# Optimization experiments

Measured on AMD Instinct MI355X. Metric: run time of the kernel, lower is better.

## Reference

```python
import jax, jax.numpy as jnp
import numpy as np

B, N, E, D, AD = 8, 1000, 4, 64, 32  # batch, n_node, n_edge_types, state_dim, annotation_dim
W_SCALE = 0.02  # matches normal_(0.0, 0.02) init


def setup_inputs() -> dict:
    key = jax.random.key(0)
    ks = jax.random.split(key, 10)
    return {
        "prop_state": jax.random.normal(ks[0], (B, N, D), jnp.float32),
        "annotation": jax.random.normal(ks[1], (B, N, AD), jnp.float32),
        "A": jax.random.uniform(ks[2], (B, N, 2 * N * E), jnp.float32),
        "W_in": W_SCALE * jax.random.normal(ks[3], (E, D, D), jnp.float32),
        "W_out": W_SCALE * jax.random.normal(ks[4], (E, D, D), jnp.float32),
        "W_r": W_SCALE * jax.random.normal(ks[5], (D, 3 * D), jnp.float32),
        "W_z": W_SCALE * jax.random.normal(ks[6], (D, 3 * D), jnp.float32),
        "W_h": W_SCALE * jax.random.normal(ks[7], (D, 3 * D), jnp.float32),
        "Wo1": W_SCALE * jax.random.normal(ks[8], (D, D + AD), jnp.float32),
        "Wo2": W_SCALE * jax.random.normal(ks[9], (1, D), jnp.float32),
    }


def _propagate(state, A_in, A_out, W_in, W_out, W_r, W_z, W_h):
    b, n, d = state.shape
    e = W_in.shape[0]
    # per-edge-type linear transforms (torch Linear: y = x @ W.T), batched over edge types
    # layout matches torch: stack over e then transpose(0,1) -> [b, e, n, d] -> [b, e*n, d]
    s_in = jnp.einsum('bnd,efd->benf', state, W_in).reshape(b, e * n, d)
    s_out = jnp.einsum('bnd,efd->benf', state, W_out).reshape(b, e * n, d)
    a_in = jnp.matmul(A_in, s_in)    # [b, n, d]
    a_out = jnp.matmul(A_out, s_out)  # [b, n, d]
    a = jnp.concatenate([a_in, a_out, state], axis=2)  # [b, n, 3d]
    r = jax.nn.sigmoid(a @ W_r.T)
    z = jax.nn.sigmoid(a @ W_z.T)
    joined = jnp.concatenate([a_in, a_out, r * state], axis=2)
    h_hat = jnp.tanh(joined @ W_h.T)
    return (1.0 - z) * state + z * h_hat


def reference(prop_state, annotation, A, W_in, W_out, W_r, W_z, W_h, Wo1, Wo2):
    n = prop_state.shape[1]
    e = W_in.shape[0]
    ne = n * e
    A_in, A_out = A[:, :, :ne], A[:, :, ne:]
    # exactly two propagation steps (n_steps_flag path in the original)
    s1 = _propagate(prop_state, A_in, A_out, W_in, W_out, W_r, W_z, W_h)
    s2 = _propagate(s1, A_in, A_out, W_in, W_out, W_r, W_z, W_h)
    join_state = jnp.concatenate([s2, annotation], axis=2)  # [b, n, d+ad]
    out = jnp.tanh(join_state @ Wo1.T) @ Wo2.T  # [b, n, 1]
    return out.sum(axis=2)  # [b, n]
```

## Files before the change

### kernel.cpp

```cpp
#include <hip/hip_runtime.h>


typedef float  f32x4_t  __attribute__((ext_vector_type(4)));
typedef __bf16 bf16x8_t __attribute__((ext_vector_type(8)));
typedef __bf16 bf16x4_t __attribute__((ext_vector_type(4)));

#define MFMA16(a, b, c) __builtin_amdgcn_mfma_f32_16x16x32_bf16((a), (b), (c), 0, 0, 0)

static constexpr int kN   = 1000;
static constexpr int kD   = 64;
static constexpr int kAD  = 32;
static constexpr int kPb  = 8000 * 64;
static constexpr int kPl  = 5;

__device__ __forceinline__ float4 ld4(const float* p) {
    return *reinterpret_cast<const float4*>(p);
}

__device__ __forceinline__ bf16x8_t cvt8(float4 a, float4 b) {
    bf16x8_t r;
    r[0] = (__bf16)a.x; r[1] = (__bf16)a.y; r[2] = (__bf16)a.z; r[3] = (__bf16)a.w;
    r[4] = (__bf16)b.x; r[5] = (__bf16)b.y; r[6] = (__bf16)b.z; r[7] = (__bf16)b.w;
    return r;
}

__device__ __forceinline__ bf16x8_t sum5pb(const __bf16* p) {
    float s0 = 0.f, s1 = 0.f, s2 = 0.f, s3 = 0.f;
    float s4 = 0.f, s5 = 0.f, s6 = 0.f, s7 = 0.f;
    #pragma unroll
    for (int pl = 0; pl < kPl; ++pl) {
        const bf16x8_t v = *reinterpret_cast<const bf16x8_t*>(p + (size_t)pl * kPb);
        s0 += (float)v[0]; s1 += (float)v[1]; s2 += (float)v[2]; s3 += (float)v[3];
        s4 += (float)v[4]; s5 += (float)v[5]; s6 += (float)v[6]; s7 += (float)v[7];
    }
    bf16x8_t r;
    r[0] = (__bf16)s0; r[1] = (__bf16)s1; r[2] = (__bf16)s2; r[3] = (__bf16)s3;
    r[4] = (__bf16)s4; r[5] = (__bf16)s5; r[6] = (__bf16)s6; r[7] = (__bf16)s7;
    return r;
}

__device__ __forceinline__ float sigm(float x) {
    x = fminf(fmaxf(x, -30.f), 30.f);
    return 1.0f / (1.0f + __expf(-x));
}

__device__ __forceinline__ float fast_tanh(float x) {
    x = fminf(fmaxf(x, -15.f), 15.f);
    const float e = __expf(-2.0f * x);
    return (1.0f - e) / (1.0f + e);
}

__global__ __launch_bounds__(256) void precompute_swt(
    const float* __restrict__ state,
    const float* __restrict__ W_in,
    const float* __restrict__ W_out,
    __bf16* __restrict__ SWTfrag)
{
    const int bx = blockIdx.x;
    const int jt = bx & 15;
    const int e  = (bx >> 4) & 3;
    const int h  = (bx >> 6) & 1;
    const int b  = bx >> 7;
    const float* W = (h ? W_out : W_in) + e * kD * kD;

    const int tid  = threadIdx.x;
    const int w    = tid >> 6;
    const int lane = tid & 63;
    const int m    = lane & 15;
    const int q    = lane >> 4;

    __shared__ __bf16 T[64][72];

    const int  jj    = jt * 64 + w * 16 + m;
    const bool valid = (jj < kN);
    const float* srow = state + ((size_t)b * kN + (valid ? jj : kN - 1)) * kD + q * 8;
    float4 a0 = ld4(srow),      a1 = ld4(srow + 4);
    float4 a2 = ld4(srow + 32), a3 = ld4(srow + 36);
    if (!valid) {
        a0 = make_float4(0.f, 0.f, 0.f, 0.f); a1 = a0; a2 = a0; a3 = a0;
    }
    const bf16x8_t af0 = cvt8(a0, a1);
    const bf16x8_t af1 = cvt8(a2, a3);

    #pragma unroll
    for (int c = 0; c < 4; ++c) {
        const int f = c * 16 + m;
        const float* wrow = W + f * kD + q * 8;
        const bf16x8_t bf0 = cvt8(ld4(wrow),      ld4(wrow + 4));
        const bf16x8_t bf1 = cvt8(ld4(wrow + 32), ld4(wrow + 36));
        f32x4_t acc = {0.f, 0.f, 0.f, 0.f};
        acc = MFMA16(af0, bf0, acc);
        acc = MFMA16(af1, bf1, acc);
        const int j0 = w * 16 + q * 4;
        bf16x4_t v;
        v[0] = (__bf16)acc[0]; v[1] = (__bf16)acc[1];
        v[2] = (__bf16)acc[2]; v[3] = (__bf16)acc[3];
        *reinterpret_cast<bf16x4_t*>(&T[f][j0]) = v;
    }
    __syncthreads();

    const int bh = b * 2 + h;
    #pragma unroll
    for (int rep = 0; rep < 2; ++rep) {
        const int m2 = tid & 15;
        const int cc = (tid >> 4) & 3;
        const int ol = (tid >> 6) + rep * 4;
        const int j0 = jt * 64 + ol * 8;
        if (j0 < kN) {
            const int jg = e * kN + j0;
            const int s  = jg >> 5;
            const int qq = (jg >> 3) & 3;
            const uint4 v = *reinterpret_cast<uint4*>(&T[cc * 16 + m2][ol * 8]);
            const size_t el = ((((size_t)bh * 125 + s) * 4 + cc) * 64 + qq * 16 + m2) * 8;
            *reinterpret_cast<uint4*>((__bf16*)SWTfrag + el) = v;
        }
    }
}

__global__ __launch_bounds__(256, 4) void fused_mm1(
    const float* __restrict__ A,
    const __bf16* __restrict__ SWTfrag,
    __bf16* __restrict__ Afrag,
    __bf16* __restrict__ a_in_p,
    __bf16* __restrict__ a_out_p)
{
    const int bx   = blockIdx.x;
    const int tile = bx & 15;
    const int rest = bx >> 4;
    const int kseg = rest % 5;
    const int rhb  = rest / 5;
    const int h    = rhb & 1;
    const int b    = rhb >> 1;

    const int t    = threadIdx.x;
    const int wv   = t >> 6;
    const int lane = t & 63;
    const int m    = lane & 15;
    const int q    = lane >> 4;

    __shared__ __bf16 L[2][64][136];

    const float* Abase = A + (size_t)b * kN * 8000 + h * 4000;
    const int bh = b * 2 + h;

    f32x4_t acc0 = {0.f, 0.f, 0.f, 0.f};
    f32x4_t acc1 = {0.f, 0.f, 0.f, 0.f};
    f32x4_t acc2 = {0.f, 0.f, 0.f, 0.f};
    f32x4_t acc3 = {0.f, 0.f, 0.f, 0.f};

    const __bf16* pBbase = SWTfrag + (size_t)bh * 125 * 2048 + (size_t)lane * 8;
    __bf16* pAout = Afrag +
        ((((size_t)(bh * 64 + tile * 4 + wv)) * 125) * 64 + lane) * 8;

    float4 ra[4][2];

    auto load_chunk = [&](int c, bool tail) {
        const int kabs = kseg * 800 + c * 128;
        #pragma unroll
        for (int p = 0; p < 4; ++p) {
            if (p == 0 || !tail) {
                const int idx = p * 256 + t;
                const int r   = tail ? (t >> 2) : (idx >> 4);
                const int c8  = tail ? (t & 3)  : (idx & 15);
                int i = tile * 64 + r;
                if (i >= kN) i = kN - 1;
                const float* src = Abase + (size_t)i * 8000 + kabs + c8 * 8;
                ra[p][0] = ld4(src);
                ra[p][1] = ld4(src + 4);
            }
        }
    };
    auto write_chunk = [&](int buf, bool tail) {
        #pragma unroll
        for (int p = 0; p < 4; ++p) {
            if (p == 0 || !tail) {
                const int idx = p * 256 + t;
                const int r   = tail ? (t >> 2) : (idx >> 4);
                const int c8  = tail ? (t & 3)  : (idx & 15);
                *reinterpret_cast<bf16x8_t*>(&L[buf][r][c8 * 8]) =
                    cvt8(ra[p][0], ra[p][1]);
            }
        }
    };
    auto compute_chunk = [&](int c, int nst, int buf) {
        #pragma unroll
        for (int sp = 0; sp < 4; ++sp) {
            if (sp < nst) {
                const int s = kseg * 25 + c * 4 + sp;
                const bf16x8_t af =
                    *reinterpret_cast<const bf16x8_t*>(&L[buf][wv * 16 + m][sp * 32 + q * 8]);
                *reinterpret_cast<bf16x8_t*>(pAout + (size_t)s * 512) = af;

                const __bf16* pB = pBbase + (size_t)s * 2048;
                const bf16x8_t b0 = *(const bf16x8_t*)(pB);
                const bf16x8_t b1 = *(const bf16x8_t*)(pB + 512);
                const bf16x8_t b2 = *(const bf16x8_t*)(pB + 1024);
                const bf16x8_t b3 = *(const bf16x8_t*)(pB + 1536);
                acc0 = MFMA16(af, b0, acc0);
                acc1 = MFMA16(af, b1, acc1);
                acc2 = MFMA16(af, b2, acc2);
                acc3 = MFMA16(af, b3, acc3);
            }
        }
    };

    load_chunk(0, false);
    write_chunk(0, false);
    __syncthreads();
    load_chunk(1, false);

    #pragma unroll 1
    for (int c = 0; c < 6; ++c) {
        compute_chunk(c, 4, c & 1);
        write_chunk((c + 1) & 1, c + 1 == 6);
        __syncthreads();
        if (c < 5)
            load_chunk(c + 2, c + 2 == 6);
    }
    compute_chunk(6, 1, 0);

    __bf16* Tw = &L[0][wv * 16][64];
    #pragma unroll
    for (int r = 0; r < 4; ++r) {
        const int row = q * 4 + r;
        Tw[row * 136 + m]      = (__bf16)acc0[r];
        Tw[row * 136 + 16 + m] = (__bf16)acc1[r];
        Tw[row * 136 + 32 + m] = (__bf16)acc2[r];
        Tw[row * 136 + 48 + m] = (__bf16)acc3[r];
    }
    __bf16* dstb = (h ? a_out_p : a_in_p) + (size_t)kseg * kPb + (size_t)b * kN * kD;
    const int ibase = tile * 64 + wv * 16;
    #pragma unroll
    for (int p2 = 0; p2 < 2; ++p2) {
        const int jr = p2 * 8 + (lane >> 3);
        const int c8 = lane & 7;
        const int i  = ibase + jr;
        if (i < kN) {
            const bf16x8_t v = *reinterpret_cast<const bf16x8_t*>(&Tw[jr * 136 + c8 * 8]);
            *reinterpret_cast<bf16x8_t*>(dstb + (size_t)i * kD + c8 * 8) = v;
        }
    }
}

__global__ __launch_bounds__(256, 4) void big_mm_f(
    const __bf16* __restrict__ Afrag,
    const __bf16* __restrict__ SWTfrag,
    __bf16* __restrict__ a_in_p,
    __bf16* __restrict__ a_out_p)
{
    const int bx   = blockIdx.x;
    const int tile = bx & 15;
    const int h    = (bx >> 4) & 1;
    const int b    = (bx >> 5) & 7;
    const int ksp  = bx >> 8;
    const int t    = threadIdx.x;
    const int wv   = t >> 6;
    const int lane = t & 63;
    const int m    = lane & 15;
    const int q    = lane >> 4;

    __shared__ __bf16 T[4][16][72];

    const int s0 = ksp * 25;
    const int ns = 25;

    const int bh = b * 2 + h;
    const __bf16* pA = Afrag +
        ((((size_t)(bh * 64 + tile * 4 + wv)) * 125 + s0) * 64 + lane) * 8;
    const __bf16* pB = SWTfrag +
        (((size_t)bh * 125 + s0) * 4 * 64) * 8 + (size_t)lane * 8;

    f32x4_t acc0 = {0.f, 0.f, 0.f, 0.f};
    f32x4_t acc1 = {0.f, 0.f, 0.f, 0.f};
    f32x4_t acc2 = {0.f, 0.f, 0.f, 0.f};
    f32x4_t acc3 = {0.f, 0.f, 0.f, 0.f};

    bf16x8_t cA  = *(const bf16x8_t*)(pA);
    bf16x8_t cB0 = *(const bf16x8_t*)(pB);
    bf16x8_t cB1 = *(const bf16x8_t*)(pB + 512);
    bf16x8_t cB2 = *(const bf16x8_t*)(pB + 1024);
    bf16x8_t cB3 = *(const bf16x8_t*)(pB + 1536);

    for (int s = 0; s < ns; ++s) {
        const int adv = (s + 1 < ns) ? 1 : 0;
        pA += adv * 512;
        pB += adv * 2048;
        const bf16x8_t nA  = *(const bf16x8_t*)(pA);
        const bf16x8_t nB0 = *(const bf16x8_t*)(pB);
        const bf16x8_t nB1 = *(const bf16x8_t*)(pB + 512);
        const bf16x8_t nB2 = *(const bf16x8_t*)(pB + 1024);
        const bf16x8_t nB3 = *(const bf16x8_t*)(pB + 1536);

        acc0 = MFMA16(cA, cB0, acc0);
        acc1 = MFMA16(cA, cB1, acc1);
        acc2 = MFMA16(cA, cB2, acc2);
        acc3 = MFMA16(cA, cB3, acc3);

        cA = nA; cB0 = nB0; cB1 = nB1; cB2 = nB2; cB3 = nB3;
    }

    #pragma unroll
    for (int r = 0; r < 4; ++r) {
        const int row = q * 4 + r;
        T[wv][row][m]      = (__bf16)acc0[r];
        T[wv][row][16 + m] = (__bf16)acc1[r];
        T[wv][row][32 + m] = (__bf16)acc2[r];
        T[wv][row][48 + m] = (__bf16)acc3[r];
    }
    __bf16* dstb = (h ? a_out_p : a_in_p) + (size_t)ksp * kPb + (size_t)b * kN * kD;
    const int ibase = tile * 64 + wv * 16;
    #pragma unroll
    for (int p2 = 0; p2 < 2; ++p2) {
        const int jr = p2 * 8 + (lane >> 3);
        const int c8 = lane & 7;
        const int i  = ibase + jr;
        if (i < kN) {
            const bf16x8_t v = *reinterpret_cast<const bf16x8_t*>(&T[wv][jr][c8 * 8]);
            *reinterpret_cast<bf16x8_t*>(dstb + (size_t)i * kD + c8 * 8) = v;
        }
    }
}

__global__ __launch_bounds__(256, 2) void gating(
    const __bf16* __restrict__ a_in_p,
    const __bf16* __restrict__ a_out_p,
    const float* __restrict__ state,
    const float* __restrict__ W_r,
    const float* __restrict__ W_z,
    const float* __restrict__ W_h,
    float* __restrict__ s_next,
    const float* __restrict__ W_in,
    const float* __restrict__ W_out,
    __bf16* __restrict__ SWTfrag,
    const float* __restrict__ ann,
    const float* __restrict__ Wo1,
    const float* __restrict__ Wo2,
    float* __restrict__ out,
    const int step)
{
    const int i0   = blockIdx.x * 16;
    const int tid  = threadIdx.x;
    const int c    = tid >> 6;
    const int lane = tid & 63;
    const int m    = lane & 15;
    const int q    = lane >> 4;
    const int f    = c * 16 + m;

    __shared__ __bf16 TL[16][72];
    __shared__ float  Osum[4][16];

    const size_t rowA = (size_t)(i0 + m);

    bf16x8_t xf[6];
    {
        const __bf16* p = a_in_p + rowA * kD + q * 8;
        xf[0] = sum5pb(p);
        xf[1] = sum5pb(p + 32);
        p = a_out_p + rowA * kD + q * 8;
        xf[2] = sum5pb(p);
        xf[3] = sum5pb(p + 32);
        const float* ps = state + rowA * kD + q * 8;
        xf[4] = cvt8(ld4(ps),      ld4(ps + 4));
        xf[5] = cvt8(ld4(ps + 32), ld4(ps + 36));
    }

    f32x4_t accr = {0.f, 0.f, 0.f, 0.f};
    f32x4_t accz = {0.f, 0.f, 0.f, 0.f};
    f32x4_t acch = {0.f, 0.f, 0.f, 0.f};

    const float* wr = W_r + f * 192 + q * 8;
    const float* wz = W_z + f * 192 + q * 8;
    const float* wh = W_h + f * 192 + q * 8;
    #pragma unroll
    for (int kc = 0; kc < 6; ++kc) {
        accr = MFMA16(xf[kc], cvt8(ld4(wr + kc * 32), ld4(wr + kc * 32 + 4)), accr);
        accz = MFMA16(xf[kc], cvt8(ld4(wz + kc * 32), ld4(wz + kc * 32 + 4)), accz);
        if (kc < 4)
            acch = MFMA16(xf[kc], cvt8(ld4(wh + kc * 32), ld4(wh + kc * 32 + 4)), acch);
    }

    float sC[4];
    #pragma unroll
    for (int r = 0; r < 4; ++r)
        sC[r] = state[(size_t)(i0 + q * 4 + r) * kD + f];

    #pragma unroll
    for (int r = 0; r < 4; ++r)
        TL[q * 4 + r][f] = (__bf16)(sigm(accr[r]) * sC[r]);
    __syncthreads();
    const bf16x8_t rs0 = *(const bf16x8_t*)&TL[m][q * 8];
    const bf16x8_t rs1 = *(const bf16x8_t*)&TL[m][32 + q * 8];

    const float* wh3 = W_h + f * 192 + 128 + q * 8;
    acch = MFMA16(rs0, cvt8(ld4(wh3),      ld4(wh3 + 4)),  acch);
    acch = MFMA16(rs1, cvt8(ld4(wh3 + 32), ld4(wh3 + 36)), acch);

    float ns[4];
    #pragma unroll
    for (int r = 0; r < 4; ++r) {
        const float zv = sigm(accz[r]);
        ns[r] = (1.f - zv) * sC[r] + zv * fast_tanh(acch[r]);
    }

    if (step == 1) {
        #pragma unroll
        for (int r = 0; r < 4; ++r)
            s_next[(size_t)(i0 + q * 4 + r) * kD + f] = ns[r];

        __syncthreads();
        #pragma unroll
        for (int r = 0; r < 4; ++r)
            TL[q * 4 + r][f] = (__bf16)ns[r];
        __syncthreads();
        const bf16x8_t sj0 = *(const bf16x8_t*)&TL[m][q * 8];
        const bf16x8_t sj1 = *(const bf16x8_t*)&TL[m][32 + q * 8];

        const int row0 = i0 + q * 4;
        const int bb   = row0 / 1000;
        const int jj0  = row0 - bb * 1000;

        #pragma unroll
        for (int u = 0; u < 2; ++u) {
            const int eh = c * 2 + u;
            const int hh = eh >> 2;
            const int ee = eh & 3;
            const float* W = (hh ? W_out : W_in) + ee * kD * kD;
            const int jg0 = ee * 1000 + jj0;
            const int s   = jg0 >> 5;
            const int qq  = (jg0 >> 3) & 3;
            const int jo  = jg0 & 7;
            const int bh2 = bb * 2 + hh;
            #pragma unroll
            for (int fg = 0; fg < 4; ++fg) {
                const int fp = fg * 16 + m;
                const float* wrow = W + fp * kD + q * 8;
                const bf16x8_t bf0 = cvt8(ld4(wrow),      ld4(wrow + 4));
                const bf16x8_t bf1 = cvt8(ld4(wrow + 32), ld4(wrow + 36));
                f32x4_t acc = {0.f, 0.f, 0.f, 0.f};
                acc = MFMA16(sj0, bf0, acc);
                acc = MFMA16(sj1, bf1, acc);
                bf16x4_t v;
                v[0] = (__bf16)acc[0]; v[1] = (__bf16)acc[1];
                v[2] = (__bf16)acc[2]; v[3] = (__bf16)acc[3];
                const size_t el =
                    ((((size_t)bh2 * 125 + s) * 4 + fg) * 64 + qq * 16 + m) * 8 + jo;
                *reinterpret_cast<bf16x4_t*>(SWTfrag + el) = v;
            }
        }
    } else {
        __syncthreads();
        #pragma unroll
        for (int r = 0; r < 4; ++r)
            TL[q * 4 + r][f] = (__bf16)ns[r];
        __syncthreads();
        const bf16x8_t j0 = *(const bf16x8_t*)&TL[m][q * 8];
        const bf16x8_t j1 = *(const bf16x8_t*)&TL[m][32 + q * 8];
        const float* ap = ann + rowA * kAD + q * 8;
        const bf16x8_t j2 = cvt8(ld4(ap), ld4(ap + 4));

        f32x4_t acco = {0.f, 0.f, 0.f, 0.f};
        const float* wo = Wo1 + (size_t)f * 96 + q * 8;
        acco = MFMA16(j0, cvt8(ld4(wo),      ld4(wo + 4)),  acco);
        acco = MFMA16(j1, cvt8(ld4(wo + 32), ld4(wo + 36)), acco);
        acco = MFMA16(j2, cvt8(ld4(wo + 64), ld4(wo + 68)), acco);

        const float w2 = Wo2[f];
        float vs[4];
        #pragma unroll
        for (int r = 0; r < 4; ++r)
            vs[r] = fast_tanh(acco[r]) * w2;
        #pragma unroll
        for (int off = 1; off <= 8; off <<= 1) {
            #pragma unroll
            for (int r = 0; r < 4; ++r)
                vs[r] += __shfl_xor(vs[r], off, 64);
        }
        if (m == 0) {
            #pragma unroll
            for (int r = 0; r < 4; ++r)
                Osum[c][q * 4 + r] = vs[r];
        }
        __syncthreads();
        if (tid < 16)
            out[i0 + tid] = Osum[0][tid] + Osum[1][tid] + Osum[2][tid] + Osum[3][tid];
    }
}

extern "C" void kernel_launch(void* const* d_in, const int* in_sizes, int n_in,
                              void* d_out, int out_size, void* d_ws, size_t ws_size,
                              hipStream_t stream) {
    (void)in_sizes; (void)n_in; (void)out_size; (void)ws_size;

    const float* prop_state = (const float*)d_in[0];
    const float* annotation = (const float*)d_in[1];
    const float* A          = (const float*)d_in[2];
    const float* W_in       = (const float*)d_in[3];
    const float* W_out      = (const float*)d_in[4];
    const float* W_r        = (const float*)d_in[5];
    const float* W_z        = (const float*)d_in[6];
    const float* W_h        = (const float*)d_in[7];
    const float* Wo1        = (const float*)d_in[8];
    const float* Wo2        = (const float*)d_in[9];
    float* out = (float*)d_out;

    char* ws = (char*)d_ws;
    __bf16* Afrag   = (__bf16*)(ws);
    __bf16* SWTfrag = (__bf16*)(ws + 131072000);
    __bf16* a_in_p  = (__bf16*)(ws + 139264000);
    __bf16* a_out_p = (__bf16*)(ws + 144384000);
    float*  s1      = (float*)(ws + 149504000);

    precompute_swt<<<1024, 256, 0, stream>>>(prop_state, W_in, W_out, SWTfrag);
    fused_mm1<<<1280, 256, 0, stream>>>(A, SWTfrag, Afrag, a_in_p, a_out_p);
    gating<<<500, 256, 0, stream>>>(a_in_p, a_out_p, prop_state, W_r, W_z, W_h,
                                    s1, W_in, W_out, SWTfrag,
                                    nullptr, nullptr, nullptr, nullptr, 1);
    big_mm_f<<<1280, 256, 0, stream>>>(Afrag, SWTfrag, a_in_p, a_out_p);
    gating<<<500, 256, 0, stream>>>(a_in_p, a_out_p, s1, W_r, W_z, W_h,
                                    nullptr, nullptr, nullptr, nullptr,
                                    annotation, Wo1, Wo2, out, 2);
}
```

Baseline: 481.7 us.

## Drop register-prefetch double buffering in fused_mm1 for higher occupancy

Replaces the double-buffered LDS tile and register prefetch of the next A chunk with a single LDS buffer that is loaded, converted and stored synchronously between two barriers. Launch bounds rise from 4 to 5 blocks per CU for fused_mm1 and big_mm_f. The goal is lower register and LDS use so more waves can hide memory latency. The cost is that global loads no longer overlap with MFMA compute inside a block, and each chunk now needs an extra barrier.

```diff
diff --git a/kernel.cpp b/kernel.cpp
--- a/kernel.cpp
+++ b/kernel.cpp
@@ -117,7 +117,7 @@
     }
 }
 
-__global__ __launch_bounds__(256, 4) void fused_mm1(
+__global__ __launch_bounds__(256, 5) void fused_mm1(
     const float* __restrict__ A,
     const __bf16* __restrict__ SWTfrag,
     __bf16* __restrict__ Afrag,
@@ -138,7 +138,7 @@
     const int m    = lane & 15;
     const int q    = lane >> 4;
 
-    __shared__ __bf16 L[2][64][136];
+    __shared__ __bf16 L[64][136];
 
     const float* Abase = A + (size_t)b * kN * 8000 + h * 4000;
     const int bh = b * 2 + h;
@@ -152,9 +152,7 @@
     __bf16* pAout = Afrag +
         ((((size_t)(bh * 64 + tile * 4 + wv)) * 125) * 64 + lane) * 8;
 
-    float4 ra[4][2];
-
-    auto load_chunk = [&](int c, bool tail) {
+    auto stage_chunk = [&](int c, bool tail) {
         const int kabs = kseg * 800 + c * 128;
         #pragma unroll
         for (int p = 0; p < 4; ++p) {
@@ -165,30 +163,18 @@
                 int i = tile * 64 + r;
                 if (i >= kN) i = kN - 1;
                 const float* src = Abase + (size_t)i * 8000 + kabs + c8 * 8;
-                ra[p][0] = ld4(src);
-                ra[p][1] = ld4(src + 4);
+                *reinterpret_cast<bf16x8_t*>(&L[r][c8 * 8]) =
+                    cvt8(ld4(src), ld4(src + 4));
             }
         }
     };
-    auto write_chunk = [&](int buf, bool tail) {
-        #pragma unroll
-        for (int p = 0; p < 4; ++p) {
-            if (p == 0 || !tail) {
-                const int idx = p * 256 + t;
-                const int r   = tail ? (t >> 2) : (idx >> 4);
-                const int c8  = tail ? (t & 3)  : (idx & 15);
-                *reinterpret_cast<bf16x8_t*>(&L[buf][r][c8 * 8]) =
-                    cvt8(ra[p][0], ra[p][1]);
-            }
-        }
-    };
-    auto compute_chunk = [&](int c, int nst, int buf) {
+    auto compute_chunk = [&](int c, int nst) {
         #pragma unroll
         for (int sp = 0; sp < 4; ++sp) {
             if (sp < nst) {
                 const int s = kseg * 25 + c * 4 + sp;
                 const bf16x8_t af =
-                    *reinterpret_cast<const bf16x8_t*>(&L[buf][wv * 16 + m][sp * 32 + q * 8]);
+                    *reinterpret_cast<const bf16x8_t*>(&L[wv * 16 + m][sp * 32 + q * 8]);
                 *reinterpret_cast<bf16x8_t*>(pAout + (size_t)s * 512) = af;
 
                 const __bf16* pB = pBbase + (size_t)s * 2048;
@@ -204,22 +190,18 @@
         }
     };
 
-    load_chunk(0, false);
-    write_chunk(0, false);
+    stage_chunk(0, false);
     __syncthreads();
-    load_chunk(1, false);
-
     #pragma unroll 1
     for (int c = 0; c < 6; ++c) {
-        compute_chunk(c, 4, c & 1);
-        write_chunk((c + 1) & 1, c + 1 == 6);
-        __syncthreads();
-        if (c < 5)
-            load_chunk(c + 2, c + 2 == 6);
-    }
-    compute_chunk(6, 1, 0);
-
-    __bf16* Tw = &L[0][wv * 16][64];
+        compute_chunk(c, 4);
+        __syncthreads();
+        stage_chunk(c + 1, c + 1 == 6);
+        __syncthreads();
+    }
+    compute_chunk(6, 1);
+
+    __bf16* Tw = &L[wv * 16][64];
     #pragma unroll
     for (int r = 0; r < 4; ++r) {
         const int row = q * 4 + r;
@@ -242,7 +224,7 @@
     }
 }
 
-__global__ __launch_bounds__(256, 4) void big_mm_f(
+__global__ __launch_bounds__(256, 5) void big_mm_f(
     const __bf16* __restrict__ Afrag,
     const __bf16* __restrict__ SWTfrag,
     __bf16* __restrict__ a_in_p,
```

Result: no change. 479.9 us (-0.4%).
